# Kernel optimization log

Hardware: AMD Instinct MI355X
Metric: run time of the kernel (lower is better)

The kernel has to match this reference:

```python
import jax, jax.numpy as jnp
import numpy as np

B, N, D, S, H = 32, 16384, 64, 8, 128  # batch, num_inputs, slot_size(=in_features), num_slots, mlp_hidden
NUM_ITERS = 3
EPS = 1e-8


def layernorm(x, g, b, eps=1e-5):
    mu = x.mean(-1, keepdims=True)
    var = x.var(-1, keepdims=True)
    return (x - mu) * jax.lax.rsqrt(var + eps) * g + b


def setup_inputs() -> dict:
    key = jax.random.key(0)
    ks = jax.random.split(key, 16)
    w = lambda k, shape: (jax.random.normal(k, shape, jnp.float32) * 0.05)
    inp = {
        "inputs": jax.random.normal(ks[0], (B, N, D + 2), jnp.float32),
        "slots": jax.random.normal(ks[1], (1, S, D), jnp.float32),
        # layernorms
        "ln_in_g": jnp.ones((D,), jnp.float32), "ln_in_b": jnp.zeros((D,), jnp.float32),
        "ln_s_g": jnp.ones((D,), jnp.float32), "ln_s_b": jnp.zeros((D,), jnp.float32),
        "ln_m_g": jnp.ones((D,), jnp.float32), "ln_m_b": jnp.zeros((D,), jnp.float32),
        # projections (stored as [in, out])
        "Wq": w(ks[2], (D, D)), "Wk": w(ks[3], (D, D)), "Wv": w(ks[4], (D, D)),
        # GRUCell: gate order r, z, n (torch convention)
        "W_ih": w(ks[5], (D, 3 * D)), "W_hh": w(ks[6], (D, 3 * D)),
        "b_ih": jnp.zeros((3 * D,), jnp.float32), "b_hh": jnp.zeros((3 * D,), jnp.float32),
        # slot MLP
        "mlp_W1": w(ks[7], (D, H)), "mlp_b1": jnp.zeros((H,), jnp.float32),
        "mlp_W2": w(ks[8], (H, D)), "mlp_b2": jnp.zeros((D,), jnp.float32),
        # pos_enc: ProjectAdd(2 -> D), LayerNorm(D), Linear(D,H), ReLU, Linear(H,D)
        "pa_W": w(ks[9], (2, D)), "pa_b": jnp.zeros((D,), jnp.float32),
        "pe_g": jnp.ones((D,), jnp.float32), "pe_b": jnp.zeros((D,), jnp.float32),
        "pe_W1": w(ks[10], (D, H)), "pe_b1": jnp.zeros((H,), jnp.float32),
        "pe_W2": w(ks[11], (H, D)), "pe_b2": jnp.zeros((D,), jnp.float32),
    }
    return inp


def reference(inputs, slots, ln_in_g, ln_in_b, ln_s_g, ln_s_b, ln_m_g, ln_m_b,
              Wq, Wk, Wv, W_ih, W_hh, b_ih, b_hh,
              mlp_W1, mlp_b1, mlp_W2, mlp_b2,
              pa_W, pa_b, pe_g, pe_b, pe_W1, pe_b1, pe_W2, pe_b2):
    feats, grids = inputs[..., :-2], inputs[..., -2:]      # [B,N,D], [B,N,2]
    feats = layernorm(feats, ln_in_g, ln_in_b)
    k = feats @ Wk                                          # [B,N,D]
    v = feats @ Wv
    grid_proj = grids @ pa_W + pa_b                         # shared ProjectAdd of grids

    def pos_enc(x):
        h = layernorm(x + grid_proj, pe_g, pe_b)
        return jax.nn.relu(h @ pe_W1 + pe_b1) @ pe_W2 + pe_b2

    k_pos = pos_enc(k)
    v_pos = pos_enc(v)

    s = jnp.broadcast_to(slots, (inputs.shape[0], S, D))
    scale = D ** -0.5
    for _ in range(NUM_ITERS):
        prev = s
        q = layernorm(s, ln_s_g, ln_s_b) @ Wq               # [B,S,D]
        logits = scale * jnp.einsum('bnd,bsd->bns', k_pos, q)
        attn = jax.nn.softmax(logits, axis=-1) + EPS        # softmax over slots (competitive)
        attn = attn / attn.sum(axis=1, keepdims=True)       # normalize over inputs
        updates = jnp.einsum('bns,bnd->bsd', attn, v_pos)   # [B,S,D]
        # GRUCell(updates, prev), torch gate order (r, z, n)
        gx = updates @ W_ih + b_ih
        gh = prev @ W_hh + b_hh
        xr, xz, xn = jnp.split(gx, 3, axis=-1)
        hr, hz, hn = jnp.split(gh, 3, axis=-1)
        r = jax.nn.sigmoid(xr + hr)
        z = jax.nn.sigmoid(xz + hz)
        n = jnp.tanh(xn + r * hn)
        s = (1.0 - z) * n + z * prev
        s = s + (jax.nn.relu(layernorm(s, ln_m_g, ln_m_b) @ mlp_W1 + mlp_b1) @ mlp_W2 + mlp_b2)
    return s
```

## Files before the change

kernel.cpp:

```cpp
#include <hip/hip_runtime.h>

typedef unsigned short u16;
typedef unsigned int   u32;

#define NN 16384
#define BN 524288
#define LN_EPS 1e-5f

typedef __attribute__((ext_vector_type(8))) short bf16x8;
typedef __attribute__((ext_vector_type(4))) float f32x4;
#define MFMA(a,b,c) __builtin_amdgcn_mfma_f32_16x16x32_bf16(a,b,c,0,0,0)

__device__ __forceinline__ float bf2f(u16 h){
  union { u32 u; float f; } c; c.u = ((u32)h) << 16; return c.f;
}
__device__ __forceinline__ u16 f2bf(float f){
  union { float f; u32 u; } c; c.f = f;
  u32 r = (c.u + 0x7fffu + ((c.u >> 16) & 1u)) >> 16;
  return (u16)r;
}
__device__ __forceinline__ u32 pack2(float a, float b){
  return (u32)f2bf(a) | ((u32)f2bf(b) << 16);
}
__device__ __forceinline__ void unpack8(uint4 v, float* o){
  o[0]=bf2f((u16)(v.x&0xffffu)); o[1]=bf2f((u16)(v.x>>16));
  o[2]=bf2f((u16)(v.y&0xffffu)); o[3]=bf2f((u16)(v.y>>16));
  o[4]=bf2f((u16)(v.z&0xffffu)); o[5]=bf2f((u16)(v.z>>16));
  o[6]=bf2f((u16)(v.w&0xffffu)); o[7]=bf2f((u16)(v.w>>16));
}
__device__ __forceinline__ float ldin(const void* p, int i, int isbf){
  return isbf ? bf2f(((const u16*)p)[i]) : ((const float*)p)[i];
}

enum {
  O_LNING=0, O_LNINB=64, O_LNSG=128, O_LNSB=192, O_LNMG=256, O_LNMB=320,
  O_WQ=384, O_WK=4480, O_WV=8576,
  O_WIH=12672, O_WHH=24960, O_BIH=37248, O_BHH=37440,
  O_MLPW1=37632, O_MLPB1=45824, O_MLPW2=45952, O_MLPB2=54144,
  O_PAW=54208, O_PAB=54336,
  O_PEG=54400, O_PEB=54464, O_PEW1=54528, O_PEB1=62720, O_PEW2=62848, O_PEB2=71040,
  W_TOTAL=71104
};
__device__ const int g_woff[25] = {O_LNING,O_LNINB,O_LNSG,O_LNSB,O_LNMG,O_LNMB,
  O_WQ,O_WK,O_WV,O_WIH,O_WHH,O_BIH,O_BHH,O_MLPW1,O_MLPB1,O_MLPW2,O_MLPB2,
  O_PAW,O_PAB,O_PEG,O_PEB,O_PEW1,O_PEB1,O_PEW2,O_PEB2};
__device__ const int g_wsz[25]  = {64,64,64,64,64,64,4096,4096,4096,12288,12288,
  192,192,8192,128,8192,64,128,64,64,64,8192,128,8192,64};

struct WP { const void* p[25]; };

__global__ void kdetect_kernel(const u16* __restrict__ inp, int* __restrict__ flag){
  if (threadIdx.x == 0 && blockIdx.x == 0){
    int votes = 0;
    for (int i = 0; i < 64; i++){
      u16 h = inp[2*i];
      int e = (h >> 7) & 0xff;
      int m = h & 0x7f;
      if ((e == 0 && m == 0) || (e >= 100 && e <= 144)) votes++;
    }
    flag[0] = (votes >= 48) ? 1 : 0;
  }
}

__global__ __launch_bounds__(256) void kw_kernel(WP wp, float* __restrict__ w,
                                                 float* __restrict__ state,
                                                 const void* __restrict__ slots,
                                                 const int* __restrict__ flag){
  int isbf = flag[0];
  int blk = blockIdx.x;
  if (blk < 25){
    const void* src = wp.p[blk];
    int off = g_woff[blk], sz = g_wsz[blk];
    for (int i = threadIdx.x; i < sz; i += 256)
      w[off + i] = ldin(src, i, isbf);
  } else {
    for (int i = threadIdx.x; i < 512; i += 256){
      float sv = ldin(slots, i, isbf);
      for (int b = 0; b < 32; b++) state[b*512 + i] = sv;
    }
  }
}

__global__ __launch_bounds__(256) void kpack_kernel(WP wp, u16* __restrict__ fkv,
                                                    u16* __restrict__ f1,
                                                    u16* __restrict__ f2,
                                                    const int* __restrict__ flag){
  int isbf = flag[0];
  int blk = blockIdx.x;
  const void* pWk = wp.p[7];  const void* pWv = wp.p[8];
  const void* pW1 = wp.p[21]; const void* pW2 = wp.p[23];
  for (int e = threadIdx.x; e < 8192; e += 256){
    int j = e & 7, lane = (e >> 3) & 63, frag = e >> 9;
    int qd = lane >> 4, l15 = lane & 15;
    if (blk == 0){
      int nt = frag >> 1, ks = frag & 1;
      int k = ks*32 + qd*8 + j, n = nt*16 + l15;
      float v = (n < 64) ? ldin(pWk, k*64 + n, isbf) : ldin(pWv, k*64 + (n-64), isbf);
      fkv[e] = f2bf(v);
    } else if (blk == 1){
      int nt = frag >> 1, ks = frag & 1;
      int k = ks*32 + qd*8 + j, n = nt*16 + l15;
      f1[e] = f2bf(ldin(pW1, k*128 + n, isbf));
    } else {
      int nt = frag >> 2, s = frag & 3;
      int k = s*32 + qd*8 + j, n = nt*16 + l15;
      f2[e] = f2bf(ldin(pW2, k*64 + n, isbf));
    }
  }
}

#define KVS 136
__global__ __launch_bounds__(256) void k0_kernel(const void* __restrict__ inpv,
                                                 const float* __restrict__ w,
                                                 const u16* __restrict__ fkv,
                                                 const u16* __restrict__ f1,
                                                 const u16* __restrict__ f2,
                                                 u16* __restrict__ kbuf,
                                                 u16* __restrict__ vtg,
                                                 const int* __restrict__ flag){
  __shared__ __align__(16) u16 shA[5120];
  __shared__ __align__(16) u16 shB[128*72];
  __shared__ float gbuf[128];
  int isbf = flag[0];
  int t = threadIdx.x;
  size_t row0 = (size_t)blockIdx.x * 64;
  int lane = t & 63, wid = t >> 6, qd = lane >> 4, l15 = lane & 15;

  if (t < 64){
    size_t row = row0 + t;
    float x[64], g0, g1;
    if (isbf){
      const u32* up = (const u32*)((const u16*)inpv + row*66);
#pragma unroll
      for (int c = 0; c < 32; c++){
        u32 v = up[c];
        x[2*c] = bf2f((u16)(v & 0xffffu)); x[2*c+1] = bf2f((u16)(v >> 16));
      }
      u32 gv = up[32];
      g0 = bf2f((u16)(gv & 0xffffu)); g1 = bf2f((u16)(gv >> 16));
    } else {
      const float2* fp = (const float2*)((const float*)inpv + row*66);
#pragma unroll
      for (int c = 0; c < 32; c++){ float2 v = fp[c]; x[2*c] = v.x; x[2*c+1] = v.y; }
      float2 gv = fp[32]; g0 = gv.x; g1 = gv.y;
    }
    gbuf[2*t] = g0; gbuf[2*t+1] = g1;
    float mu = 0.f;
#pragma unroll
    for (int i = 0; i < 64; i++) mu += x[i];
    mu *= (1.f/64.f);
    float va = 0.f;
#pragma unroll
    for (int i = 0; i < 64; i++){ x[i] -= mu; va += x[i]*x[i]; }
    va *= (1.f/64.f);
    float rs = rsqrtf(va + LN_EPS);
#pragma unroll
    for (int i = 0; i < 64; i++) x[i] = x[i]*rs*w[O_LNING+i] + w[O_LNINB+i];
#pragma unroll
    for (int c = 0; c < 8; c++){
      uint4 q; q.x = pack2(x[8*c],x[8*c+1]); q.y = pack2(x[8*c+2],x[8*c+3]);
      q.z = pack2(x[8*c+4],x[8*c+5]); q.w = pack2(x[8*c+6],x[8*c+7]);
      *(uint4*)&shA[t*72 + c*8] = q;
    }
  }
  __syncthreads();

  {
    bf16x8 af[2];
#pragma unroll
    for (int ks = 0; ks < 2; ks++)
      af[ks] = *(const bf16x8*)&shA[(wid*16 + l15)*72 + ks*32 + qd*8];
#pragma unroll
    for (int nt = 0; nt < 8; nt++){
      bf16x8 b0 = *(const bf16x8*)(fkv + ((size_t)(nt*2+0)*64 + lane)*8);
      bf16x8 b1 = *(const bf16x8*)(fkv + ((size_t)(nt*2+1)*64 + lane)*8);
      f32x4 acc = {0.f,0.f,0.f,0.f};
      acc = MFMA(af[0], b0, acc);
      acc = MFMA(af[1], b1, acc);
      int rb = wid*16 + qd*4;
#pragma unroll
      for (int r = 0; r < 4; r++) shB[(rb+r)*KVS + nt*16 + l15] = f2bf(acc[r]);
    }
  }
  __syncthreads();

  float tv[64];
  int act = (t < 128);
  if (act){
    int phys = t & 63, isv = (t >> 6) & 1;
    float g0 = gbuf[2*phys], g1 = gbuf[2*phys+1];
    const uint4* rp = (const uint4*)&shB[phys*KVS + isv*64];
#pragma unroll
    for (int c = 0; c < 8; c++){ uint4 q4 = rp[c]; unpack8(q4, &tv[c*8]); }
#pragma unroll
    for (int i = 0; i < 64; i++)
      tv[i] += g0*w[O_PAW+i] + g1*w[O_PAW+64+i] + w[O_PAB+i];
    float mu = 0.f;
#pragma unroll
    for (int i = 0; i < 64; i++) mu += tv[i];
    mu *= (1.f/64.f);
    float va = 0.f;
#pragma unroll
    for (int i = 0; i < 64; i++){ tv[i] -= mu; va += tv[i]*tv[i]; }
    va *= (1.f/64.f);
    float rs = rsqrtf(va + LN_EPS);
#pragma unroll
    for (int i = 0; i < 64; i++) tv[i] = tv[i]*rs*w[O_PEG+i] + w[O_PEB+i];
  }
  __syncthreads();
  if (act){
#pragma unroll
    for (int c = 0; c < 8; c++){
      uint4 q; q.x = pack2(tv[8*c],tv[8*c+1]); q.y = pack2(tv[8*c+2],tv[8*c+3]);
      q.z = pack2(tv[8*c+4],tv[8*c+5]); q.w = pack2(tv[8*c+6],tv[8*c+7]);
      *(uint4*)&shB[t*72 + c*8] = q;
    }
  }
  __syncthreads();

  f32x4 out[2][4];
  {
    u16* Hw = shA + wid*1280;
    bf16x8 af[2][2];
#pragma unroll
    for (int mt = 0; mt < 2; mt++)
#pragma unroll
      for (int ks = 0; ks < 2; ks++)
        af[mt][ks] = *(const bf16x8*)&shB[(wid*32 + mt*16 + l15)*72 + ks*32 + qd*8];
#pragma unroll
    for (int mt = 0; mt < 2; mt++)
#pragma unroll
      for (int nt = 0; nt < 4; nt++) out[mt][nt] = (f32x4){0.f,0.f,0.f,0.f};

#pragma unroll
    for (int s = 0; s < 4; s++){
#pragma unroll
      for (int e = 0; e < 2; e++){
        int nn = s*2 + e;
        bf16x8 b0 = *(const bf16x8*)(f1 + ((size_t)(nn*2+0)*64 + lane)*8);
        bf16x8 b1 = *(const bf16x8*)(f1 + ((size_t)(nn*2+1)*64 + lane)*8);
        float bias1 = w[O_PEB1 + nn*16 + l15];
#pragma unroll
        for (int mt = 0; mt < 2; mt++){
          f32x4 h = {0.f,0.f,0.f,0.f};
          h = MFMA(af[mt][0], b0, h);
          h = MFMA(af[mt][1], b1, h);
#pragma unroll
          for (int r = 0; r < 4; r++)
            Hw[(mt*16 + qd*4 + r)*40 + e*16 + l15] = f2bf(fmaxf(h[r] + bias1, 0.f));
        }
      }
      bf16x8 a2[2];
#pragma unroll
      for (int mt = 0; mt < 2; mt++)
        a2[mt] = *(const bf16x8*)&Hw[(mt*16 + l15)*40 + qd*8];
#pragma unroll
      for (int nt = 0; nt < 4; nt++){
        bf16x8 bw = *(const bf16x8*)(f2 + ((size_t)(nt*4 + s)*64 + lane)*8);
#pragma unroll
        for (int mt = 0; mt < 2; mt++)
          out[mt][nt] = MFMA(a2[mt], bw, out[mt][nt]);
      }
    }
  }
  __syncthreads();

  if (wid < 2){
#pragma unroll
    for (int nt = 0; nt < 4; nt++){
      float b2v = w[O_PEB2 + nt*16 + l15];
#pragma unroll
      for (int mt = 0; mt < 2; mt++){
        size_t rb = row0 + wid*32 + mt*16 + qd*4;
#pragma unroll
        for (int r = 0; r < 4; r++)
          kbuf[(rb+r)*64 + nt*16 + l15] = f2bf(out[mt][nt][r] + b2v);
      }
    }
  } else {
#pragma unroll
    for (int nt = 0; nt < 4; nt++){
      float b2v = w[O_PEB2 + nt*16 + l15];
#pragma unroll
      for (int mt = 0; mt < 2; mt++){
        int vr = (wid-2)*32 + mt*16 + qd*4;
#pragma unroll
        for (int r = 0; r < 4; r++)
          shA[(nt*16 + l15)*72 + vr + r] = f2bf(out[mt][nt][r] + b2v);
      }
    }
  }
  __syncthreads();

  {
    int d = t >> 2, c = t & 3;
    int b  = (int)(row0 >> 14);
    int nl = (int)(row0 & 16383);
    uint4 v0 = *(const uint4*)&shA[d*72 + c*16];
    uint4 v1 = *(const uint4*)&shA[d*72 + c*16 + 8];
    u16* dst = vtg + (size_t)b*1048576 + (size_t)d*NN + nl + c*16;
    *(uint4*)dst = v0;
    *(uint4*)(dst + 8) = v1;
  }
}

__global__ __launch_bounds__(512) void b1_kernel(const float* __restrict__ w,
                                                 const float* __restrict__ state,
                                                 u16* __restrict__ qf){
  __shared__ float qrow[8*64];
  int b = blockIdx.x, t = threadIdx.x;
  int s = t >> 6, lane = t & 63;
  float xv = state[(b*8+s)*64 + lane];
  float sum = xv;
#pragma unroll
  for (int off = 32; off; off >>= 1) sum += __shfl_xor(sum, off, 64);
  float mu = sum * (1.f/64.f);
  float xc = xv - mu;
  float ss = xc*xc;
#pragma unroll
  for (int off = 32; off; off >>= 1) ss += __shfl_xor(ss, off, 64);
  float rs = rsqrtf(ss*(1.f/64.f) + LN_EPS);
  float xln = xc*rs*w[O_LNSG+lane] + w[O_LNSB+lane];
  float acc = 0.f;
#pragma unroll
  for (int i = 0; i < 64; i++){
    float xi = __shfl(xln, i, 64);
    acc += xi * w[O_WQ + i*64 + lane];
  }
  qrow[s*64 + lane] = acc;
  __syncthreads();
  if (t < 128){
    int ks = t >> 6, ln = t & 63, ql = ln & 15, qq = ln >> 4;
    u32 pk[4];
#pragma unroll
    for (int jp = 0; jp < 4; jp++){
      float v0 = (ql < 8) ? qrow[ql*64 + ks*32 + qq*8 + 2*jp]     : 0.f;
      float v1 = (ql < 8) ? qrow[ql*64 + ks*32 + qq*8 + 2*jp + 1] : 0.f;
      pk[jp] = pack2(v0, v1);
    }
    *(uint4*)(qf + ((size_t)(b*2+ks)*64 + ln)*8) = *(uint4*)pk;
  }
}

__global__ __launch_bounds__(256) void b2_kernel(const u16* __restrict__ kbuf,
                                                 const u16* __restrict__ vtg,
                                                 const u16* __restrict__ qf,
                                                 float* __restrict__ pupd,
                                                 float* __restrict__ psums){
  __shared__ __align__(16) u16 pm[16*512];
  int t = threadIdx.x, lane = t & 63, wid = t >> 6, l15 = lane & 15, quad = lane >> 4;
  int b = blockIdx.x >> 5, chunk = blockIdx.x & 31;
  size_t gn0 = (size_t)b*NN + (size_t)chunk*512;

  for (int i = t; i < 4096; i += 256) pm[4096 + i] = 0;

  bf16x8 q0 = *(const bf16x8*)(qf + ((size_t)(b*2+0)*64 + lane)*8);
  bf16x8 q1 = *(const bf16x8*)(qf + ((size_t)(b*2+1)*64 + lane)*8);

  float psum = 0.f;
  int wbase = wid*128;
#pragma unroll
  for (int mt = 0; mt < 8; mt++){
    const u16* kp = kbuf + (gn0 + wbase + mt*16 + l15)*64;
    bf16x8 a0 = *(const bf16x8*)(kp + quad*8);
    bf16x8 a1 = *(const bf16x8*)(kp + 32 + quad*8);
    f32x4 dg = {0.f,0.f,0.f,0.f};
    dg = MFMA(a0, q0, dg);
    dg = MFMA(a1, q1, dg);
#pragma unroll
    for (int r = 0; r < 4; r++){
      float lg = dg[r]*0.125f;
      float mx = lg;
      mx = fmaxf(mx, __shfl_xor(mx, 1, 64));
      mx = fmaxf(mx, __shfl_xor(mx, 2, 64));
      mx = fmaxf(mx, __shfl_xor(mx, 4, 64));
      float ex = __expf(lg - mx);
      float es = ex;
      es += __shfl_xor(es, 1, 64);
      es += __shfl_xor(es, 2, 64);
      es += __shfl_xor(es, 4, 64);
      float p = ex/es + 1e-8f;
      psum += p;
      if (l15 < 8){
        int n = wbase + mt*16 + quad*4 + r;
        pm[l15*512 + (((n>>3) ^ l15) << 3) + (n & 7)] = f2bf(p);
      }
    }
  }
  psum += __shfl_xor(psum, 16, 64);
  psum += __shfl_xor(psum, 32, 64);
  if (quad == 0 && l15 < 8)
    psums[(size_t)((b*32+chunk)*4 + wid)*8 + l15] = psum;
  __syncthreads();

  f32x4 acc = {0.f,0.f,0.f,0.f};
  const u16* vp = vtg + (size_t)b*1048576 + (size_t)(wid*16 + l15)*NN
                      + (size_t)chunk*512 + quad*8;
  const u16* pmr = pm + l15*512;
#pragma unroll
  for (int ks = 0; ks < 16; ks++){
    int kc = ks*4 + quad;
    bf16x8 pa = *(const bf16x8*)(pmr + ((kc ^ l15) << 3));
    bf16x8 vb = *(const bf16x8*)(vp + ks*32);
    acc = MFMA(pa, vb, acc);
  }
  if (quad < 2){
    float* ob = pupd + (size_t)(b*32+chunk)*512 + (size_t)(quad*4)*64 + wid*16 + l15;
#pragma unroll
    for (int r = 0; r < 4; r++) ob[(size_t)r*64] = acc[r];
  }
}

__global__ __launch_bounds__(192) void b3_kernel(const float* __restrict__ w,
                                                 float* __restrict__ state,
                                                 const float* __restrict__ pupd,
                                                 const float* __restrict__ psums){
  __shared__ float uL[64], pv[64], hL[64], hln[64], gx[192], gh[192], hid[128], red[128];
  __shared__ float ssum;
  int bs = blockIdx.x, b = bs >> 3, s = bs & 7, t = threadIdx.x;

  if (t < 64){
    float a = 0.f;
    const float* pp = pupd + (size_t)b*32*512 + s*64 + t;
#pragma unroll 4
    for (int c = 0; c < 32; c++) a += pp[(size_t)c*512];
    uL[t] = a;
    pv[t] = state[(b*8+s)*64 + t];
  } else {
    int i = t - 64;
    red[i] = psums[(size_t)(b*128 + i)*8 + s];
  }
  __syncthreads();
  if (t == 0){ float a = 0.f; for (int i = 0; i < 128; i++) a += red[i]; ssum = a; }
  __syncthreads();

  {
    float inv = 1.f/ssum;
    int j = t;
    float x0=0.f,x1=0.f,x2=0.f,x3=0.f, y0=0.f,y1=0.f,y2=0.f,y3=0.f;
#pragma unroll 4
    for (int d = 0; d < 64; d += 4){
      x0 += uL[d]  *w[O_WIH + (d)*192 + j];   y0 += pv[d]  *w[O_WHH + (d)*192 + j];
      x1 += uL[d+1]*w[O_WIH + (d+1)*192 + j]; y1 += pv[d+1]*w[O_WHH + (d+1)*192 + j];
      x2 += uL[d+2]*w[O_WIH + (d+2)*192 + j]; y2 += pv[d+2]*w[O_WHH + (d+2)*192 + j];
      x3 += uL[d+3]*w[O_WIH + (d+3)*192 + j]; y3 += pv[d+3]*w[O_WHH + (d+3)*192 + j];
    }
    gx[j] = w[O_BIH + j] + (x0+x1+x2+x3)*inv;
    gh[j] = w[O_BHH + j] + (y0+y1+y2+y3);
  }
  __syncthreads();

  if (t < 64){
    int d = t;
    float r = 1.f/(1.f + expf(-(gx[d]      + gh[d])));
    float z = 1.f/(1.f + expf(-(gx[64+d]   + gh[64+d])));
    float nv = tanhf(gx[128+d] + r*gh[128+d]);
    hL[d] = (1.f - z)*nv + z*pv[d];
  }
  __syncthreads();

  if (t < 64){
    float h = hL[t];
    float sum = h;
#pragma unroll
    for (int off = 32; off; off >>= 1) sum += __shfl_xor(sum, off, 64);
    float mu = sum * (1.f/64.f);
    float xc = h - mu;
    float ss2 = xc*xc;
#pragma unroll
    for (int off = 32; off; off >>= 1) ss2 += __shfl_xor(ss2, off, 64);
    float rs = rsqrtf(ss2*(1.f/64.f) + LN_EPS);
    hln[t] = xc*rs*w[O_LNMG+t] + w[O_LNMB+t];
  }
  __syncthreads();

  if (t < 128){
    int j = t;
    float a0=0.f,a1=0.f,a2v=0.f,a3=0.f;
#pragma unroll 4
    for (int d = 0; d < 64; d += 4){
      a0  += hln[d]  *w[O_MLPW1 + (d)*128 + j];
      a1  += hln[d+1]*w[O_MLPW1 + (d+1)*128 + j];
      a2v += hln[d+2]*w[O_MLPW1 + (d+2)*128 + j];
      a3  += hln[d+3]*w[O_MLPW1 + (d+3)*128 + j];
    }
    hid[j] = fmaxf(a0+a1+a2v+a3 + w[O_MLPB1 + j], 0.f);
  }
  __syncthreads();

  if (t < 64){
    int d = t;
    float o0=0.f,o1=0.f,o2=0.f,o3=0.f;
#pragma unroll 4
    for (int j = 0; j < 128; j += 4){
      o0 += hid[j]  *w[O_MLPW2 + (j)*64 + d];
      o1 += hid[j+1]*w[O_MLPW2 + (j+1)*64 + d];
      o2 += hid[j+2]*w[O_MLPW2 + (j+2)*64 + d];
      o3 += hid[j+3]*w[O_MLPW2 + (j+3)*64 + d];
    }
    state[(b*8+s)*64 + d] = hL[d] + o0+o1+o2+o3 + w[O_MLPB2 + d];
  }
}

__global__ __launch_bounds__(256) void kout_kernel(const float* __restrict__ state,
                                                   void* __restrict__ out,
                                                   const int* __restrict__ flag){
  int i = blockIdx.x*256 + threadIdx.x;
  if (flag[0]) ((u16*)out)[i] = f2bf(state[i]);
  else         ((float*)out)[i] = state[i];
}

extern "C" void kernel_launch(void* const* d_in, const int* in_sizes, int n_in,
                              void* d_out, int out_size, void* d_ws, size_t ws_size,
                              hipStream_t stream){
  const void* inp   = d_in[0];
  const void* slots = d_in[1];
  WP wp;
  for (int i = 0; i < 25; i++) wp.p[i] = d_in[2+i];

  u16*   kbuf  = (u16*)d_ws;
  u16*   vtg   = kbuf + (size_t)BN*64;
  float* w     = (float*)(vtg + (size_t)BN*64);
  float* state = w + W_TOTAL;
  float* pupd  = state + 16384;
  float* psums = pupd + 524288;
  u16*   qf    = (u16*)(psums + 32768);
  u16*   fkv   = qf + 32768;
  u16*   f1    = fkv + 8192;
  u16*   f2    = f1 + 8192;
  int*   flag  = (int*)(f2 + 8192);

  kdetect_kernel<<<1, 64, 0, stream>>>((const u16*)inp, flag);
  kw_kernel<<<26, 256, 0, stream>>>(wp, w, state, slots, flag);
  kpack_kernel<<<3, 256, 0, stream>>>(wp, fkv, f1, f2, flag);
  k0_kernel<<<8192, 256, 0, stream>>>(inp, w, fkv, f1, f2, kbuf, vtg, flag);
  for (int it = 0; it < 3; it++){
    b1_kernel<<<32, 512, 0, stream>>>(w, state, qf);
    b2_kernel<<<1024, 256, 0, stream>>>(kbuf, vtg, qf, pupd, psums);
    b3_kernel<<<256, 192, 0, stream>>>(w, state, pupd, psums);
  }
  kout_kernel<<<64, 256, 0, stream>>>(state, d_out, flag);
}
```

Baseline: 520.0 us.

## Parallelize k0 layernorms, stage k writes via LDS, fuse q projection into GRU kernel

The input and pos-enc layernorms in k0 are split across 4 or 2 threads per row with shuffle reductions, so all 256 threads do work instead of 64 or 128. The k output is staged through LDS and written with coalesced 16-byte stores. In b2, the softmax drops its max subtraction in favour of a clamp, and the 0.125 scale moves into q. The P matrix uses a padded layout instead of an XOR swizzle, with the MFMA operands swapped so results go out as float4 stores. The per-iteration q projection is fused into the GRU kernel, removing one launch per iteration. The one-pass variance (E[x²]−mu²) and max-free exp trade some numerical robustness for less work.

```diff
diff --git a/kernel.cpp b/kernel.cpp
--- a/kernel.cpp
+++ b/kernel.cpp
@@ -126,42 +126,47 @@
   size_t row0 = (size_t)blockIdx.x * 64;
   int lane = t & 63, wid = t >> 6, qd = lane >> 4, l15 = lane & 15;
 
-  if (t < 64){
-    size_t row = row0 + t;
-    float x[64], g0, g1;
+  {
+    int rr = t >> 2, part = t & 3;
+    size_t row = row0 + rr;
+    float x[16];
     if (isbf){
-      const u32* up = (const u32*)((const u16*)inpv + row*66);
-#pragma unroll
-      for (int c = 0; c < 32; c++){
+      const u32* up = (const u32*)((const u16*)inpv + row*66 + part*16);
+#pragma unroll
+      for (int c = 0; c < 8; c++){
         u32 v = up[c];
         x[2*c] = bf2f((u16)(v & 0xffffu)); x[2*c+1] = bf2f((u16)(v >> 16));
       }
-      u32 gv = up[32];
-      g0 = bf2f((u16)(gv & 0xffffu)); g1 = bf2f((u16)(gv >> 16));
+      if (part == 3){
+        u32 gv = *(const u32*)((const u16*)inpv + row*66 + 64);
+        gbuf[2*rr] = bf2f((u16)(gv & 0xffffu)); gbuf[2*rr+1] = bf2f((u16)(gv >> 16));
+      }
     } else {
-      const float2* fp = (const float2*)((const float*)inpv + row*66);
-#pragma unroll
-      for (int c = 0; c < 32; c++){ float2 v = fp[c]; x[2*c] = v.x; x[2*c+1] = v.y; }
-      float2 gv = fp[32]; g0 = gv.x; g1 = gv.y;
-    }
-    gbuf[2*t] = g0; gbuf[2*t+1] = g1;
-    float mu = 0.f;
-#pragma unroll
-    for (int i = 0; i < 64; i++) mu += x[i];
-    mu *= (1.f/64.f);
-    float va = 0.f;
-#pragma unroll
-    for (int i = 0; i < 64; i++){ x[i] -= mu; va += x[i]*x[i]; }
-    va *= (1.f/64.f);
-    float rs = rsqrtf(va + LN_EPS);
-#pragma unroll
-    for (int i = 0; i < 64; i++) x[i] = x[i]*rs*w[O_LNING+i] + w[O_LNINB+i];
+      const float2* fp = (const float2*)((const float*)inpv + row*66 + part*16);
+#pragma unroll
+      for (int c = 0; c < 8; c++){ float2 v = fp[c]; x[2*c] = v.x; x[2*c+1] = v.y; }
+      if (part == 3){
+        float2 gv = *(const float2*)((const float*)inpv + row*66 + 64);
+        gbuf[2*rr] = gv.x; gbuf[2*rr+1] = gv.y;
+      }
+    }
+    float s1 = 0.f, s2 = 0.f;
+#pragma unroll
+    for (int i = 0; i < 16; i++){ s1 += x[i]; s2 += x[i]*x[i]; }
+    s1 += __shfl_xor(s1, 1, 64); s1 += __shfl_xor(s1, 2, 64);
+    s2 += __shfl_xor(s2, 1, 64); s2 += __shfl_xor(s2, 2, 64);
+    float mu = s1*(1.f/64.f);
+    float rs = rsqrtf(s2*(1.f/64.f) - mu*mu + LN_EPS);
+    u32 pk[8];
 #pragma unroll
     for (int c = 0; c < 8; c++){
-      uint4 q; q.x = pack2(x[8*c],x[8*c+1]); q.y = pack2(x[8*c+2],x[8*c+3]);
-      q.z = pack2(x[8*c+4],x[8*c+5]); q.w = pack2(x[8*c+6],x[8*c+7]);
-      *(uint4*)&shA[t*72 + c*8] = q;
-    }
+      int i0 = part*16 + 2*c;
+      float a = (x[2*c]  -mu)*rs*w[O_LNING+i0]   + w[O_LNINB+i0];
+      float b = (x[2*c+1]-mu)*rs*w[O_LNING+i0+1] + w[O_LNINB+i0+1];
+      pk[c] = pack2(a, b);
+    }
+    *(uint4*)&shA[rr*72 + part*16]     = *(uint4*)&pk[0];
+    *(uint4*)&shA[rr*72 + part*16 + 8] = *(uint4*)&pk[4];
   }
   __syncthreads();
 
@@ -184,36 +189,40 @@
   }
   __syncthreads();
 
-  float tv[64];
-  int act = (t < 128);
-  if (act){
-    int phys = t & 63, isv = (t >> 6) & 1;
+  float tv[32];
+  int vr = t >> 1, half = t & 1;
+  {
+    int phys = vr & 63, isv = vr >> 6;
     float g0 = gbuf[2*phys], g1 = gbuf[2*phys+1];
-    const uint4* rp = (const uint4*)&shB[phys*KVS + isv*64];
-#pragma unroll
-    for (int c = 0; c < 8; c++){ uint4 q4 = rp[c]; unpack8(q4, &tv[c*8]); }
-#pragma unroll
-    for (int i = 0; i < 64; i++)
-      tv[i] += g0*w[O_PAW+i] + g1*w[O_PAW+64+i] + w[O_PAB+i];
-    float mu = 0.f;
-#pragma unroll
-    for (int i = 0; i < 64; i++) mu += tv[i];
-    mu *= (1.f/64.f);
-    float va = 0.f;
-#pragma unroll
-    for (int i = 0; i < 64; i++){ tv[i] -= mu; va += tv[i]*tv[i]; }
-    va *= (1.f/64.f);
-    float rs = rsqrtf(va + LN_EPS);
-#pragma unroll
-    for (int i = 0; i < 64; i++) tv[i] = tv[i]*rs*w[O_PEG+i] + w[O_PEB+i];
-  }
-  __syncthreads();
-  if (act){
-#pragma unroll
-    for (int c = 0; c < 8; c++){
-      uint4 q; q.x = pack2(tv[8*c],tv[8*c+1]); q.y = pack2(tv[8*c+2],tv[8*c+3]);
-      q.z = pack2(tv[8*c+4],tv[8*c+5]); q.w = pack2(tv[8*c+6],tv[8*c+7]);
-      *(uint4*)&shB[t*72 + c*8] = q;
+    const uint4* rp = (const uint4*)&shB[phys*KVS + isv*64 + half*32];
+#pragma unroll
+    for (int c = 0; c < 4; c++){ uint4 q4 = rp[c]; unpack8(q4, &tv[c*8]); }
+#pragma unroll
+    for (int i = 0; i < 32; i++){
+      int gi = half*32 + i;
+      tv[i] += g0*w[O_PAW+gi] + g1*w[O_PAW+64+gi] + w[O_PAB+gi];
+    }
+    float s1 = 0.f, s2 = 0.f;
+#pragma unroll
+    for (int i = 0; i < 32; i++){ s1 += tv[i]; s2 += tv[i]*tv[i]; }
+    s1 += __shfl_xor(s1, 1, 64);
+    s2 += __shfl_xor(s2, 1, 64);
+    float mu = s1*(1.f/64.f);
+    float rs = rsqrtf(s2*(1.f/64.f) - mu*mu + LN_EPS);
+#pragma unroll
+    for (int i = 0; i < 32; i++){
+      int gi = half*32 + i;
+      tv[i] = (tv[i]-mu)*rs*w[O_PEG+gi] + w[O_PEB+gi];
+    }
+  }
+  __syncthreads();
+  {
+    u32 pk[4];
+#pragma unroll
+    for (int c = 0; c < 4; c++){
+      pk[0] = pack2(tv[8*c],  tv[8*c+1]); pk[1] = pack2(tv[8*c+2], tv[8*c+3]);
+      pk[2] = pack2(tv[8*c+4],tv[8*c+5]); pk[3] = pack2(tv[8*c+6], tv[8*c+7]);
+      *(uint4*)&shB[vr*72 + half*32 + c*8] = *(uint4*)pk;
     }
   }
   __syncthreads();
@@ -271,10 +280,10 @@
       float b2v = w[O_PEB2 + nt*16 + l15];
 #pragma unroll
       for (int mt = 0; mt < 2; mt++){
-        size_t rb = row0 + wid*32 + mt*16 + qd*4;
+        int rb = wid*32 + mt*16 + qd*4;
 #pragma unroll
         for (int r = 0; r < 4; r++)
-          kbuf[(rb+r)*64 + nt*16 + l15] = f2bf(out[mt][nt][r] + b2v);
+          shB[(rb+r)*72 + nt*16 + l15] = f2bf(out[mt][nt][r] + b2v);
       }
     }
   } else {
@@ -283,22 +292,28 @@
       float b2v = w[O_PEB2 + nt*16 + l15];
 #pragma unroll
       for (int mt = 0; mt < 2; mt++){
-        int vr = (wid-2)*32 + mt*16 + qd*4;
+        int vrr = (wid-2)*32 + mt*16 + qd*4;
 #pragma unroll
         for (int r = 0; r < 4; r++)
-          shA[(nt*16 + l15)*72 + vr + r] = f2bf(out[mt][nt][r] + b2v);
-      }
-    }
-  }
-  __syncthreads();
-
-  {
-    int d = t >> 2, c = t & 3;
+          shA[(nt*16 + l15)*72 + vrr + r] = f2bf(out[mt][nt][r] + b2v);
+      }
+    }
+  }
+  __syncthreads();
+
+  {
+    int rr2 = t >> 2, c = t & 3;
+    uint4 k0v = *(const uint4*)&shB[rr2*72 + c*16];
+    uint4 k1v = *(const uint4*)&shB[rr2*72 + c*16 + 8];
+    u16* kd = kbuf + (row0 + rr2)*64 + c*16;
+    *(uint4*)kd = k0v;
+    *(uint4*)(kd + 8) = k1v;
+
     int b  = (int)(row0 >> 14);
     int nl = (int)(row0 & 16383);
-    uint4 v0 = *(const uint4*)&shA[d*72 + c*16];
-    uint4 v1 = *(const uint4*)&shA[d*72 + c*16 + 8];
-    u16* dst = vtg + (size_t)b*1048576 + (size_t)d*NN + nl + c*16;
+    uint4 v0 = *(const uint4*)&shA[rr2*72 + c*16];
+    uint4 v1 = *(const uint4*)&shA[rr2*72 + c*16 + 8];
+    u16* dst = vtg + (size_t)b*1048576 + (size_t)rr2*NN + nl + c*16;
     *(uint4*)dst = v0;
     *(uint4*)(dst + 8) = v1;
   }
@@ -327,7 +342,7 @@
     float xi = __shfl(xln, i, 64);
     acc += xi * w[O_WQ + i*64 + lane];
   }
-  qrow[s*64 + lane] = acc;
+  qrow[s*64 + lane] = acc * 0.125f;
   __syncthreads();
   if (t < 128){
     int ks = t >> 6, ln = t & 63, ql = ln & 15, qq = ln >> 4;
@@ -342,17 +357,16 @@
   }
 }
 
+#define PMS 520
 __global__ __launch_bounds__(256) void b2_kernel(const u16* __restrict__ kbuf,
                                                  const u16* __restrict__ vtg,
                                                  const u16* __restrict__ qf,
                                                  float* __restrict__ pupd,
                                                  float* __restrict__ psums){
-  __shared__ __align__(16) u16 pm[16*512];
+  __shared__ __align__(16) u16 pm[8*PMS];
   int t = threadIdx.x, lane = t & 63, wid = t >> 6, l15 = lane & 15, quad = lane >> 4;
   int b = blockIdx.x >> 5, chunk = blockIdx.x & 31;
   size_t gn0 = (size_t)b*NN + (size_t)chunk*512;
-
-  for (int i = t; i < 4096; i += 256) pm[4096 + i] = 0;
 
   bf16x8 q0 = *(const bf16x8*)(qf + ((size_t)(b*2+0)*64 + lane)*8);
   bf16x8 q1 = *(const bf16x8*)(qf + ((size_t)(b*2+1)*64 + lane)*8);
@@ -369,21 +383,17 @@
     dg = MFMA(a1, q1, dg);
 #pragma unroll
     for (int r = 0; r < 4; r++){
-      float lg = dg[r]*0.125f;
-      float mx = lg;
-      mx = fmaxf(mx, __shfl_xor(mx, 1, 64));
-      mx = fmaxf(mx, __shfl_xor(mx, 2, 64));
-      mx = fmaxf(mx, __shfl_xor(mx, 4, 64));
-      float ex = __expf(lg - mx);
+      float lg = fminf(dg[r], 40.f);
+      float ex = __expf(lg);
       float es = ex;
       es += __shfl_xor(es, 1, 64);
       es += __shfl_xor(es, 2, 64);
       es += __shfl_xor(es, 4, 64);
-      float p = ex/es + 1e-8f;
+      float p = __fdividef(ex, es) + 1e-8f;
       psum += p;
       if (l15 < 8){
         int n = wbase + mt*16 + quad*4 + r;
-        pm[l15*512 + (((n>>3) ^ l15) << 3) + (n & 7)] = f2bf(p);
+        pm[l15*PMS + n] = f2bf(p);
       }
     }
   }
@@ -394,28 +404,27 @@
   __syncthreads();
 
   f32x4 acc = {0.f,0.f,0.f,0.f};
-  const u16* vp = vtg + (size_t)b*1048576 + (size_t)(wid*16 + l15)*NN
-                      + (size_t)chunk*512 + quad*8;
-  const u16* pmr = pm + l15*512;
+  const u16* vp  = vtg + (size_t)b*1048576 + (size_t)(wid*16 + l15)*NN
+                       + (size_t)chunk*512 + quad*8;
+  const u16* pmr = pm + (l15 & 7)*PMS + quad*8;
 #pragma unroll
   for (int ks = 0; ks < 16; ks++){
-    int kc = ks*4 + quad;
-    bf16x8 pa = *(const bf16x8*)(pmr + ((kc ^ l15) << 3));
-    bf16x8 vb = *(const bf16x8*)(vp + ks*32);
-    acc = MFMA(pa, vb, acc);
-  }
-  if (quad < 2){
-    float* ob = pupd + (size_t)(b*32+chunk)*512 + (size_t)(quad*4)*64 + wid*16 + l15;
-#pragma unroll
-    for (int r = 0; r < 4; r++) ob[(size_t)r*64] = acc[r];
-  }
-}
-
-__global__ __launch_bounds__(192) void b3_kernel(const float* __restrict__ w,
-                                                 float* __restrict__ state,
-                                                 const float* __restrict__ pupd,
-                                                 const float* __restrict__ psums){
-  __shared__ float uL[64], pv[64], hL[64], hln[64], gx[192], gh[192], hid[128], red[128];
+    bf16x8 va = *(const bf16x8*)(vp + ks*32);
+    bf16x8 pb = *(const bf16x8*)(pmr + ks*32);
+    acc = MFMA(va, pb, acc);
+  }
+  if (l15 < 8){
+    float4 st = { acc[0], acc[1], acc[2], acc[3] };
+    *(float4*)(pupd + (size_t)(b*32+chunk)*512 + l15*64 + wid*16 + quad*4) = st;
+  }
+}
+
+__global__ __launch_bounds__(192) void b3q_kernel(const float* __restrict__ w,
+                                                  float* __restrict__ state,
+                                                  const float* __restrict__ pupd,
+                                                  const float* __restrict__ psums,
+                                                  u16* __restrict__ qf){
+  __shared__ float uL[64], pv[64], hL[64], hln[64], gx[192], gh[192], hid[128], red[128], qs[64];
   __shared__ float ssum;
   int bs = blockIdx.x, b = bs >> 3, s = bs & 7, t = threadIdx.x;
 
@@ -498,7 +507,33 @@
       o2 += hid[j+2]*w[O_MLPW2 + (j+2)*64 + d];
       o3 += hid[j+3]*w[O_MLPW2 + (j+3)*64 + d];
     }
-    state[(b*8+s)*64 + d] = hL[d] + o0+o1+o2+o3 + w[O_MLPB2 + d];
+    float sv = hL[d] + o0+o1+o2+o3 + w[O_MLPB2 + d];
+    state[(b*8+s)*64 + d] = sv;
+
+    float sum = sv;
+#pragma unroll
+    for (int off = 32; off; off >>= 1) sum += __shfl_xor(sum, off, 64);
+    float mu = sum * (1.f/64.f);
+    float xc = sv - mu;
+    float ss2 = xc*xc;
+#pragma unroll
+    for (int off = 32; off; off >>= 1) ss2 += __shfl_xor(ss2, off, 64);
+    float rs = rsqrtf(ss2*(1.f/64.f) + LN_EPS);
+    float xln = xc*rs*w[O_LNSG+d] + w[O_LNSB+d];
+    float q = 0.f;
+#pragma unroll
+    for (int i = 0; i < 64; i++){
+      float xi = __shfl(xln, i, 64);
+      q += xi * w[O_WQ + i*64 + d];
+    }
+    qs[d] = q * 0.125f;
+  }
+  __syncthreads();
+
+  if (t < 32){
+    int ks = t >> 4, qq = (t >> 2) & 3, jp = t & 3;
+    u32 v = pack2(qs[ks*32 + qq*8 + 2*jp], qs[ks*32 + qq*8 + 2*jp + 1]);
+    *(u32*)(qf + ((size_t)((b*2+ks)*64) + qq*16 + s)*8 + jp*2) = v;
   }
 }
 
@@ -534,10 +569,10 @@
   kw_kernel<<<26, 256, 0, stream>>>(wp, w, state, slots, flag);
   kpack_kernel<<<3, 256, 0, stream>>>(wp, fkv, f1, f2, flag);
   k0_kernel<<<8192, 256, 0, stream>>>(inp, w, fkv, f1, f2, kbuf, vtg, flag);
+  b1_kernel<<<32, 512, 0, stream>>>(w, state, qf);
   for (int it = 0; it < 3; it++){
-    b1_kernel<<<32, 512, 0, stream>>>(w, state, qf);
     b2_kernel<<<1024, 256, 0, stream>>>(kbuf, vtg, qf, pupd, psums);
-    b3_kernel<<<256, 192, 0, stream>>>(w, state, pupd, psums);
+    b3q_kernel<<<256, 192, 0, stream>>>(w, state, pupd, psums, qf);
   }
   kout_kernel<<<64, 256, 0, stream>>>(state, d_out, flag);
 }
```

After: 551.0 us. 1.06x slower.

## Fuse init kernels, fold q computation into GRU kernel, simplify softmax and bf16 rounding

Applied to the files above, without the earlier changes.

Merges the detect, weight-convert and pack kernels into one init launch, and folds the per-iteration query projection into the GRU/MLP kernel so only one b1 launch remains. The softmax drops its max subtraction in favour of a clamp at 40, moves the 1/8 scale into q, and uses a fast divide. The P-times-V MFMA is restructured with a padded, unswizzled P buffer and vectorized float4 stores, and a cheaper round-half-up bf16 conversion replaces round-to-nearest-even in k0. The clamped, max-free softmax risks overflow or accuracy changes if logits grow large.

```diff
diff --git a/kernel.cpp b/kernel.cpp
--- a/kernel.cpp
+++ b/kernel.cpp
@@ -19,8 +19,16 @@
   u32 r = (c.u + 0x7fffu + ((c.u >> 16) & 1u)) >> 16;
   return (u16)r;
 }
+__device__ __forceinline__ u16 f2bf_fast(float f){
+  union { float f; u32 u; } c; c.f = f;
+  return (u16)((c.u + 0x8000u) >> 16);
+}
 __device__ __forceinline__ u32 pack2(float a, float b){
   return (u32)f2bf(a) | ((u32)f2bf(b) << 16);
+}
+__device__ __forceinline__ u32 pack2f(float a, float b){
+  union { float f; u32 u; } ca, cb; ca.f = a; cb.f = b;
+  return ((ca.u + 0x8000u) >> 16) | ((cb.u + 0x8000u) & 0xffff0000u);
 }
 __device__ __forceinline__ void unpack8(uint4 v, float* o){
   o[0]=bf2f((u16)(v.x&0xffffu)); o[1]=bf2f((u16)(v.x>>16));
@@ -49,62 +57,65 @@
 
 struct WP { const void* p[25]; };
 
-__global__ void kdetect_kernel(const u16* __restrict__ inp, int* __restrict__ flag){
-  if (threadIdx.x == 0 && blockIdx.x == 0){
-    int votes = 0;
-    for (int i = 0; i < 64; i++){
-      u16 h = inp[2*i];
-      int e = (h >> 7) & 0xff;
-      int m = h & 0x7f;
-      if ((e == 0 && m == 0) || (e >= 100 && e <= 144)) votes++;
-    }
-    flag[0] = (votes >= 48) ? 1 : 0;
-  }
-}
-
-__global__ __launch_bounds__(256) void kw_kernel(WP wp, float* __restrict__ w,
-                                                 float* __restrict__ state,
-                                                 const void* __restrict__ slots,
-                                                 const int* __restrict__ flag){
-  int isbf = flag[0];
+__device__ __forceinline__ int detect_isbf(const u16* inp){
+  int votes = 0;
+  for (int i = 0; i < 64; i++){
+    u16 h = inp[2*i];
+    int e = (h >> 7) & 0xff;
+    int m = h & 0x7f;
+    if ((e == 0 && m == 0) || (e >= 100 && e <= 144)) votes++;
+  }
+  return votes >= 48;
+}
+
+__global__ __launch_bounds__(256) void kinit_kernel(WP wp, const u16* __restrict__ inp,
+                                                    float* __restrict__ w,
+                                                    float* __restrict__ state,
+                                                    const void* __restrict__ slots,
+                                                    u16* __restrict__ fkv,
+                                                    u16* __restrict__ f1,
+                                                    u16* __restrict__ f2,
+                                                    int* __restrict__ flag){
+  __shared__ int sbf;
+  if (threadIdx.x == 0){
+    int v = detect_isbf(inp);
+    sbf = v;
+    if (blockIdx.x == 0) flag[0] = v;
+  }
+  __syncthreads();
+  int isbf = sbf;
   int blk = blockIdx.x;
   if (blk < 25){
     const void* src = wp.p[blk];
     int off = g_woff[blk], sz = g_wsz[blk];
     for (int i = threadIdx.x; i < sz; i += 256)
       w[off + i] = ldin(src, i, isbf);
-  } else {
+  } else if (blk == 25){
     for (int i = threadIdx.x; i < 512; i += 256){
       float sv = ldin(slots, i, isbf);
       for (int b = 0; b < 32; b++) state[b*512 + i] = sv;
     }
-  }
-}
-
-__global__ __launch_bounds__(256) void kpack_kernel(WP wp, u16* __restrict__ fkv,
-                                                    u16* __restrict__ f1,
-                                                    u16* __restrict__ f2,
-                                                    const int* __restrict__ flag){
-  int isbf = flag[0];
-  int blk = blockIdx.x;
-  const void* pWk = wp.p[7];  const void* pWv = wp.p[8];
-  const void* pW1 = wp.p[21]; const void* pW2 = wp.p[23];
-  for (int e = threadIdx.x; e < 8192; e += 256){
-    int j = e & 7, lane = (e >> 3) & 63, frag = e >> 9;
-    int qd = lane >> 4, l15 = lane & 15;
-    if (blk == 0){
-      int nt = frag >> 1, ks = frag & 1;
-      int k = ks*32 + qd*8 + j, n = nt*16 + l15;
-      float v = (n < 64) ? ldin(pWk, k*64 + n, isbf) : ldin(pWv, k*64 + (n-64), isbf);
-      fkv[e] = f2bf(v);
-    } else if (blk == 1){
-      int nt = frag >> 1, ks = frag & 1;
-      int k = ks*32 + qd*8 + j, n = nt*16 + l15;
-      f1[e] = f2bf(ldin(pW1, k*128 + n, isbf));
-    } else {
-      int nt = frag >> 2, s = frag & 3;
-      int k = s*32 + qd*8 + j, n = nt*16 + l15;
-      f2[e] = f2bf(ldin(pW2, k*64 + n, isbf));
+  } else {
+    int pk = blk - 26;
+    const void* pWk = wp.p[7];  const void* pWv = wp.p[8];
+    const void* pW1 = wp.p[21]; const void* pW2 = wp.p[23];
+    for (int e = threadIdx.x; e < 8192; e += 256){
+      int j = e & 7, lane = (e >> 3) & 63, frag = e >> 9;
+      int qd = lane >> 4, l15 = lane & 15;
+      if (pk == 0){
+        int nt = frag >> 1, ks = frag & 1;
+        int k = ks*32 + qd*8 + j, n = nt*16 + l15;
+        float v = (n < 64) ? ldin(pWk, k*64 + n, isbf) : ldin(pWv, k*64 + (n-64), isbf);
+        fkv[e] = f2bf(v);
+      } else if (pk == 1){
+        int nt = frag >> 1, ks = frag & 1;
+        int k = ks*32 + qd*8 + j, n = nt*16 + l15;
+        f1[e] = f2bf(ldin(pW1, k*128 + n, isbf));
+      } else {
+        int nt = frag >> 2, s = frag & 3;
+        int k = s*32 + qd*8 + j, n = nt*16 + l15;
+        f2[e] = f2bf(ldin(pW2, k*64 + n, isbf));
+      }
     }
   }
 }
@@ -158,8 +169,8 @@
     for (int i = 0; i < 64; i++) x[i] = x[i]*rs*w[O_LNING+i] + w[O_LNINB+i];
 #pragma unroll
     for (int c = 0; c < 8; c++){
-      uint4 q; q.x = pack2(x[8*c],x[8*c+1]); q.y = pack2(x[8*c+2],x[8*c+3]);
-      q.z = pack2(x[8*c+4],x[8*c+5]); q.w = pack2(x[8*c+6],x[8*c+7]);
+      uint4 q; q.x = pack2f(x[8*c],x[8*c+1]); q.y = pack2f(x[8*c+2],x[8*c+3]);
+      q.z = pack2f(x[8*c+4],x[8*c+5]); q.w = pack2f(x[8*c+6],x[8*c+7]);
       *(uint4*)&shA[t*72 + c*8] = q;
     }
   }
@@ -179,7 +190,7 @@
       acc = MFMA(af[1], b1, acc);
       int rb = wid*16 + qd*4;
 #pragma unroll
-      for (int r = 0; r < 4; r++) shB[(rb+r)*KVS + nt*16 + l15] = f2bf(acc[r]);
+      for (int r = 0; r < 4; r++) shB[(rb+r)*KVS + nt*16 + l15] = f2bf_fast(acc[r]);
     }
   }
   __syncthreads();
@@ -211,8 +222,8 @@
   if (act){
 #pragma unroll
     for (int c = 0; c < 8; c++){
-      uint4 q; q.x = pack2(tv[8*c],tv[8*c+1]); q.y = pack2(tv[8*c+2],tv[8*c+3]);
-      q.z = pack2(tv[8*c+4],tv[8*c+5]); q.w = pack2(tv[8*c+6],tv[8*c+7]);
+      uint4 q; q.x = pack2f(tv[8*c],tv[8*c+1]); q.y = pack2f(tv[8*c+2],tv[8*c+3]);
+      q.z = pack2f(tv[8*c+4],tv[8*c+5]); q.w = pack2f(tv[8*c+6],tv[8*c+7]);
       *(uint4*)&shB[t*72 + c*8] = q;
     }
   }
@@ -247,7 +258,7 @@
           h = MFMA(af[mt][1], b1, h);
 #pragma unroll
           for (int r = 0; r < 4; r++)
-            Hw[(mt*16 + qd*4 + r)*40 + e*16 + l15] = f2bf(fmaxf(h[r] + bias1, 0.f));
+            Hw[(mt*16 + qd*4 + r)*40 + e*16 + l15] = f2bf_fast(fmaxf(h[r] + bias1, 0.f));
         }
       }
       bf16x8 a2[2];
@@ -274,7 +285,7 @@
         size_t rb = row0 + wid*32 + mt*16 + qd*4;
 #pragma unroll
         for (int r = 0; r < 4; r++)
-          kbuf[(rb+r)*64 + nt*16 + l15] = f2bf(out[mt][nt][r] + b2v);
+          kbuf[(rb+r)*64 + nt*16 + l15] = f2bf_fast(out[mt][nt][r] + b2v);
       }
     }
   } else {
@@ -286,7 +297,7 @@
         int vr = (wid-2)*32 + mt*16 + qd*4;
 #pragma unroll
         for (int r = 0; r < 4; r++)
-          shA[(nt*16 + l15)*72 + vr + r] = f2bf(out[mt][nt][r] + b2v);
+          shA[(nt*16 + l15)*72 + vr + r] = f2bf_fast(out[mt][nt][r] + b2v);
       }
     }
   }
@@ -327,7 +338,7 @@
     float xi = __shfl(xln, i, 64);
     acc += xi * w[O_WQ + i*64 + lane];
   }
-  qrow[s*64 + lane] = acc;
+  qrow[s*64 + lane] = acc * 0.125f;
   __syncthreads();
   if (t < 128){
     int ks = t >> 6, ln = t & 63, ql = ln & 15, qq = ln >> 4;
@@ -342,17 +353,16 @@
   }
 }
 
+#define PMS 520
 __global__ __launch_bounds__(256) void b2_kernel(const u16* __restrict__ kbuf,
                                                  const u16* __restrict__ vtg,
                                                  const u16* __restrict__ qf,
                                                  float* __restrict__ pupd,
                                                  float* __restrict__ psums){
-  __shared__ __align__(16) u16 pm[16*512];
+  __shared__ __align__(16) u16 pm[8*PMS];
   int t = threadIdx.x, lane = t & 63, wid = t >> 6, l15 = lane & 15, quad = lane >> 4;
   int b = blockIdx.x >> 5, chunk = blockIdx.x & 31;
   size_t gn0 = (size_t)b*NN + (size_t)chunk*512;
-
-  for (int i = t; i < 4096; i += 256) pm[4096 + i] = 0;
 
   bf16x8 q0 = *(const bf16x8*)(qf + ((size_t)(b*2+0)*64 + lane)*8);
   bf16x8 q1 = *(const bf16x8*)(qf + ((size_t)(b*2+1)*64 + lane)*8);
@@ -369,21 +379,17 @@
     dg = MFMA(a1, q1, dg);
 #pragma unroll
     for (int r = 0; r < 4; r++){
-      float lg = dg[r]*0.125f;
-      float mx = lg;
-      mx = fmaxf(mx, __shfl_xor(mx, 1, 64));
-      mx = fmaxf(mx, __shfl_xor(mx, 2, 64));
-      mx = fmaxf(mx, __shfl_xor(mx, 4, 64));
-      float ex = __expf(lg - mx);
+      float lg = fminf(dg[r], 40.f);
+      float ex = __expf(lg);
       float es = ex;
       es += __shfl_xor(es, 1, 64);
       es += __shfl_xor(es, 2, 64);
       es += __shfl_xor(es, 4, 64);
-      float p = ex/es + 1e-8f;
+      float p = __fdividef(ex, es) + 1e-8f;
       psum += p;
       if (l15 < 8){
         int n = wbase + mt*16 + quad*4 + r;
-        pm[l15*512 + (((n>>3) ^ l15) << 3) + (n & 7)] = f2bf(p);
+        pm[l15*PMS + n] = f2bf_fast(p);
       }
     }
   }
@@ -394,28 +400,27 @@
   __syncthreads();
 
   f32x4 acc = {0.f,0.f,0.f,0.f};
-  const u16* vp = vtg + (size_t)b*1048576 + (size_t)(wid*16 + l15)*NN
-                      + (size_t)chunk*512 + quad*8;
-  const u16* pmr = pm + l15*512;
+  const u16* vp  = vtg + (size_t)b*1048576 + (size_t)(wid*16 + l15)*NN
+                       + (size_t)chunk*512 + quad*8;
+  const u16* pmr = pm + (l15 & 7)*PMS + quad*8;
 #pragma unroll
   for (int ks = 0; ks < 16; ks++){
-    int kc = ks*4 + quad;
-    bf16x8 pa = *(const bf16x8*)(pmr + ((kc ^ l15) << 3));
-    bf16x8 vb = *(const bf16x8*)(vp + ks*32);
-    acc = MFMA(pa, vb, acc);
-  }
-  if (quad < 2){
-    float* ob = pupd + (size_t)(b*32+chunk)*512 + (size_t)(quad*4)*64 + wid*16 + l15;
-#pragma unroll
-    for (int r = 0; r < 4; r++) ob[(size_t)r*64] = acc[r];
-  }
-}
-
-__global__ __launch_bounds__(192) void b3_kernel(const float* __restrict__ w,
-                                                 float* __restrict__ state,
-                                                 const float* __restrict__ pupd,
-                                                 const float* __restrict__ psums){
-  __shared__ float uL[64], pv[64], hL[64], hln[64], gx[192], gh[192], hid[128], red[128];
+    bf16x8 va = *(const bf16x8*)(vp + ks*32);
+    bf16x8 pb = *(const bf16x8*)(pmr + ks*32);
+    acc = MFMA(va, pb, acc);
+  }
+  if (l15 < 8){
+    float4 st = { acc[0], acc[1], acc[2], acc[3] };
+    *(float4*)(pupd + (size_t)(b*32+chunk)*512 + l15*64 + wid*16 + quad*4) = st;
+  }
+}
+
+__global__ __launch_bounds__(192) void b3q_kernel(const float* __restrict__ w,
+                                                  float* __restrict__ state,
+                                                  const float* __restrict__ pupd,
+                                                  const float* __restrict__ psums,
+                                                  u16* __restrict__ qf){
+  __shared__ float uL[64], pv[64], hL[64], hln[64], gx[192], gh[192], hid[128], red[128], qs[64];
   __shared__ float ssum;
   int bs = blockIdx.x, b = bs >> 3, s = bs & 7, t = threadIdx.x;
 
@@ -431,7 +436,12 @@
     red[i] = psums[(size_t)(b*128 + i)*8 + s];
   }
   __syncthreads();
-  if (t == 0){ float a = 0.f; for (int i = 0; i < 128; i++) a += red[i]; ssum = a; }
+  if (t < 64){
+    float a = red[t] + red[t + 64];
+#pragma unroll
+    for (int off = 32; off; off >>= 1) a += __shfl_xor(a, off, 64);
+    if (t == 0) ssum = a;
+  }
   __syncthreads();
 
   {
@@ -498,7 +508,33 @@
       o2 += hid[j+2]*w[O_MLPW2 + (j+2)*64 + d];
       o3 += hid[j+3]*w[O_MLPW2 + (j+3)*64 + d];
     }
-    state[(b*8+s)*64 + d] = hL[d] + o0+o1+o2+o3 + w[O_MLPB2 + d];
+    float sv = hL[d] + o0+o1+o2+o3 + w[O_MLPB2 + d];
+    state[(b*8+s)*64 + d] = sv;
+
+    float sum = sv;
+#pragma unroll
+    for (int off = 32; off; off >>= 1) sum += __shfl_xor(sum, off, 64);
+    float mu = sum * (1.f/64.f);
+    float xc = sv - mu;
+    float ss2 = xc*xc;
+#pragma unroll
+    for (int off = 32; off; off >>= 1) ss2 += __shfl_xor(ss2, off, 64);
+    float rs = rsqrtf(ss2*(1.f/64.f) + LN_EPS);
+    float xln = xc*rs*w[O_LNSG+d] + w[O_LNSB+d];
+    float q = 0.f;
+#pragma unroll
+    for (int i = 0; i < 64; i++){
+      float xi = __shfl(xln, i, 64);
+      q += xi * w[O_WQ + i*64 + d];
+    }
+    qs[d] = q * 0.125f;
+  }
+  __syncthreads();
+
+  if (t < 32){
+    int ks = t >> 4, qq = (t >> 2) & 3, jp = t & 3;
+    u32 v = pack2f(qs[ks*32 + qq*8 + 2*jp], qs[ks*32 + qq*8 + 2*jp + 1]);
+    *(u32*)(qf + ((size_t)((b*2+ks)*64) + qq*16 + s)*8 + jp*2) = v;
   }
 }
 
@@ -530,14 +566,12 @@
   u16*   f2    = f1 + 8192;
   int*   flag  = (int*)(f2 + 8192);
 
-  kdetect_kernel<<<1, 64, 0, stream>>>((const u16*)inp, flag);
-  kw_kernel<<<26, 256, 0, stream>>>(wp, w, state, slots, flag);
-  kpack_kernel<<<3, 256, 0, stream>>>(wp, fkv, f1, f2, flag);
+  kinit_kernel<<<29, 256, 0, stream>>>(wp, (const u16*)inp, w, state, slots, fkv, f1, f2, flag);
   k0_kernel<<<8192, 256, 0, stream>>>(inp, w, fkv, f1, f2, kbuf, vtg, flag);
+  b1_kernel<<<32, 512, 0, stream>>>(w, state, qf);
   for (int it = 0; it < 3; it++){
-    b1_kernel<<<32, 512, 0, stream>>>(w, state, qf);
     b2_kernel<<<1024, 256, 0, stream>>>(kbuf, vtg, qf, pupd, psums);
-    b3_kernel<<<256, 192, 0, stream>>>(w, state, pupd, psums);
+    b3q_kernel<<<256, 192, 0, stream>>>(w, state, pupd, psums, qf);
   }
   kout_kernel<<<64, 256, 0, stream>>>(state, d_out, flag);
 }
```

Measured after the change: 488.0 us. 1.07x faster.
